# Kernel tuning notes

Hardware: AMD Instinct MI355X
Metric: run time of the kernel (lower is better)

## Reference

```python
import jax, jax.numpy as jnp
import numpy as np

HEADS = 20
HEAD_DIM = 64
NUM_IP = 20          # num_content_tokens (4) + num_style_tokens (16)
FU_SCALE = 0.5
STYLE_SCALE = 1.0
SCALE = 1.0 / np.sqrt(HEAD_DIM).astype(np.float32)


def setup_inputs() -> dict:
    key = jax.random.key(0)
    ks = jax.random.split(key, 9)
    B, S, H, C = 4, 4096, 1280, 2048
    T = 77 + NUM_IP  # text tokens + ip tokens
    w = 0.02
    return {
        "hidden_states": jax.random.normal(ks[0], (B, S, H), jnp.float32),
        "encoder_hidden_states": jax.random.normal(ks[1], (B, T, C), jnp.float32),
        "Wq": jax.random.normal(ks[2], (H, H), jnp.float32) * w,
        "Wk": jax.random.normal(ks[3], (H, C), jnp.float32) * w,
        "Wv": jax.random.normal(ks[4], (H, C), jnp.float32) * w,
        "Wk_ip": jax.random.normal(ks[5], (H, C), jnp.float32) * w,
        "Wv_ip": jax.random.normal(ks[6], (H, C), jnp.float32) * w,
        "Wo": jax.random.normal(ks[7], (H, H), jnp.float32) * w,
        "bo": jnp.zeros((H,), jnp.float32),
    }


def _to_heads(x):
    # [B, T, H] -> [B, heads, T, head_dim]
    B, T, _ = x.shape
    return x.reshape(B, T, HEADS, HEAD_DIM).transpose(0, 2, 1, 3)


def _blend(p):
    # cross-batch prob fusion: rows 1<-0, 3<-2 (CFG pairs)
    p = p.at[1].set(FU_SCALE * p[1] + (1.0 - FU_SCALE) * p[0])
    p = p.at[3].set(FU_SCALE * p[3] + (1.0 - FU_SCALE) * p[2])
    return p


def reference(hidden_states, encoder_hidden_states, Wq, Wk, Wv, Wk_ip, Wv_ip, Wo, bo):
    B, S, H = hidden_states.shape
    text = encoder_hidden_states[:, :-NUM_IP, :]   # [B, 77, C]
    ip = encoder_hidden_states[:, -NUM_IP:, :]     # [B, 20, C]

    q = _to_heads(hidden_states @ Wq.T)            # [B, h, S, d]
    k = _to_heads(text @ Wk.T)                     # [B, h, 77, d]
    v = _to_heads(text @ Wv.T)

    # fuAttn branch: explicit probs, blended across batch, then PV matmul
    probs = jax.nn.softmax(jnp.einsum('bhqd,bhkd->bhqk', q, k) * SCALE, axis=-1)
    probs = _blend(probs)
    raw = jnp.einsum('bhqk,bhkd->bhqd', probs, v)
    raw = raw.transpose(0, 2, 1, 3).reshape(B, S, H)

    # IP-adapter style cross-attention (fuIPAttn branch)
    ip_k = _to_heads(ip @ Wk_ip.T)                 # [B, h, 20, d]
    ip_v = _to_heads(ip @ Wv_ip.T)
    ip_probs = jax.nn.softmax(jnp.einsum('bhqd,bhkd->bhqk', q, ip_k) * SCALE, axis=-1)
    ip_probs = _blend(ip_probs)
    ip_hs = jnp.einsum('bhqk,bhkd->bhqd', ip_probs, ip_v)
    ip_hs = ip_hs.transpose(0, 2, 1, 3).reshape(B, S, H)

    hs = raw + STYLE_SCALE * ip_hs
    # batch rows 0 and 2 keep raw (text-only) attention output
    hs = hs.at[0].set(raw[0]).at[2].set(raw[2])

    # to_out[0] linear (bias) + to_out[1] dropout (identity at inference)
    return hs @ Wo.T + bo
```

## Files before the change

### kernel.cpp

```cpp
#include <hip/hip_runtime.h>
#include <cstdint>

typedef float floatx4 __attribute__((ext_vector_type(4)));
typedef __bf16 bf16x8 __attribute__((ext_vector_type(8)));

typedef const __attribute__((address_space(1))) void* gas_cvp;
typedef __attribute__((address_space(3))) void* las_vp;

__device__ __forceinline__ float bflo(unsigned int u) {
    return __builtin_bit_cast(float, u << 16);
}
__device__ __forceinline__ float bfhi(unsigned int u) {
    return __builtin_bit_cast(float, u & 0xffff0000u);
}
__device__ __forceinline__ unsigned short f2bf(float f) {
    unsigned int u = __builtin_bit_cast(unsigned int, f);
    u += 0x7fffu + ((u >> 16) & 1u);
    return (unsigned short)(u >> 16);
}
__device__ __forceinline__ bf16x8 ld8(const unsigned short* p) {
    return __builtin_bit_cast(bf16x8, *(const uint4*)p);
}
__device__ __forceinline__ floatx4 mfma32(bf16x8 a, bf16x8 b, floatx4 c) {
    return __builtin_amdgcn_mfma_f32_16x16x32_bf16(a, b, c, 0, 0, 0);
}
__device__ __forceinline__ void load_lds16(const void* g, void* l) {
    __builtin_amdgcn_global_load_lds(
        (gas_cvp)(unsigned long long)g,
        (las_vp)(unsigned int)(unsigned long long)l,
        16, 0, 0);
}

__global__ void cvt_f32_bf16(const float* __restrict__ in,
                             unsigned short* __restrict__ out, int n4) {
    int i = blockIdx.x * 256 + threadIdx.x;
    if (i < n4) {
        float4 v = ((const float4*)in)[i];
        ushort4 o;
        o.x = f2bf(v.x); o.y = f2bf(v.y); o.z = f2bf(v.z); o.w = f2bf(v.w);
        ((ushort4*)out)[i] = o;
    }
}

struct GemmJob {
    const unsigned short* A;
    const unsigned short* B;
    void* C;
    int M, N, K;
    int rpb, bstride, roff;
};
struct GemmArgs { GemmJob j[4]; };

template <bool F32OUT>
__global__ __launch_bounds__(256, 2) void gemm_bt(GemmArgs args,
                                                  const float* __restrict__ bias) {
    GemmJob jb = args.j[blockIdx.z];
    const int ntiles = jb.N >> 7;
    const int mtiles = (jb.M + 127) >> 7;

    int bx, by;
    {
        int idx = blockIdx.x;
        if ((mtiles & 7) == 0) {
            int gsz = ntiles * 8;
            int group = idx / gsz;
            int rem = idx - group * gsz;
            by = group * 8 + (rem & 7);
            bx = rem >> 3;
        } else {
            by = idx / ntiles;
            bx = idx - by * ntiles;
        }
    }
    if (by * 128 >= jb.M) return;

    const int tid  = threadIdx.x;
    const int lane = tid & 63;
    const int wid  = tid >> 6;
    const int K = jb.K, N = jb.N;

    __shared__ unsigned short ldsA[128 * 32];
    __shared__ unsigned short ldsB[128 * 32];

    const int colA = (tid & 3) * 8;
    auto maprow = [&](int r) -> size_t {
        r = (r < jb.M) ? r : (jb.M - 1);
        int b = r / jb.rpb;
        int t = r - b * jb.rpb;
        return (size_t)(b * jb.bstride + jb.roff + t);
    };
    const unsigned short* pa0 = jb.A + maprow(by * 128 + (tid >> 2)) * K + colA;
    const unsigned short* pa1 = jb.A + maprow(by * 128 + 64 + (tid >> 2)) * K + colA;
    const unsigned short* pb0 = jb.B + (size_t)(bx * 128 + (tid >> 2)) * K + colA;
    const unsigned short* pb1 = jb.B + (size_t)(bx * 128 + 64 + (tid >> 2)) * K + colA;

    unsigned short* la0 = &ldsA[tid * 8];
    unsigned short* la1 = &ldsA[2048 + tid * 8];
    unsigned short* lb0 = &ldsB[tid * 8];
    unsigned short* lb1 = &ldsB[2048 + tid * 8];

    floatx4 acc[4][4] = {};

    const int wm = (wid & 1) * 64;
    const int wn = (wid >> 1) * 64;
    const int fr = lane & 15;
    const int fc = (lane >> 4) * 8;

    for (int k0 = 0; k0 < K; k0 += 32) {
        __syncthreads();
        load_lds16(pa0 + k0, la0);
        load_lds16(pa1 + k0, la1);
        load_lds16(pb0 + k0, lb0);
        load_lds16(pb1 + k0, lb1);
        __syncthreads();

        bf16x8 af[4], bfv[4];
#pragma unroll
        for (int i = 0; i < 4; i++)
            af[i] = *(const bf16x8*)&ldsA[(wm + i * 16 + fr) * 32 + fc];
#pragma unroll
        for (int i = 0; i < 4; i++)
            bfv[i] = *(const bf16x8*)&ldsB[(wn + i * 16 + fr) * 32 + fc];
#pragma unroll
        for (int mi = 0; mi < 4; mi++)
#pragma unroll
            for (int ni = 0; ni < 4; ni++)
                acc[mi][ni] = __builtin_amdgcn_mfma_f32_16x16x32_bf16(
                    af[mi], bfv[ni], acc[mi][ni], 0, 0, 0);
    }

    const int colBase = bx * 128 + wn;
    const int rowBase = by * 128 + wm;
#pragma unroll
    for (int mi = 0; mi < 4; mi++) {
#pragma unroll
        for (int ni = 0; ni < 4; ni++) {
            int col  = colBase + ni * 16 + (lane & 15);
            int row0 = rowBase + mi * 16 + (lane >> 4) * 4;
#pragma unroll
            for (int r = 0; r < 4; r++) {
                int row = row0 + r;
                if (row < jb.M) {
                    float v = acc[mi][ni][r];
                    if (F32OUT)
                        ((float*)jb.C)[(size_t)row * N + col] = v + bias[col];
                    else
                        ((unsigned short*)jb.C)[(size_t)row * N + col] = f2bf(v);
                }
            }
        }
    }
}

#define NT 77
#define NI 20
#define VSTR 104
#define ISTR 40

__global__ __launch_bounds__(256, 2) void attn_mfma(
    const unsigned short* __restrict__ q,
    const unsigned short* __restrict__ kt,
    const unsigned short* __restrict__ vt,
    const unsigned short* __restrict__ kip,
    const unsigned short* __restrict__ vip,
    unsigned short* __restrict__ outp)
{
    const int tid = threadIdx.x;
    const int qt = blockIdx.x;
    const int h  = blockIdx.y;
    const int pz = blockIdx.z;
    const int b0 = 2 * pz;
    const int lane  = tid & 63;
    const int w     = tid >> 6;
    const int bi    = w >> 1;
    const int strip = (w & 1) * 16;
    const int fr = lane & 15;
    const int g  = lane >> 4;

    __shared__ unsigned short sVt[2][64][VSTR];
    __shared__ unsigned short sVipt[2][64][ISTR];
    __shared__ unsigned short sP[2][32][VSTR];

    for (int i = tid; i < 2 * 64 * (VSTR - NT); i += 256) {
        int b = i / (64 * (VSTR - NT)); int rem = i % (64 * (VSTR - NT));
        sVt[b][rem / (VSTR - NT)][NT + rem % (VSTR - NT)] = 0;
    }
    for (int i = tid; i < 2 * 64 * (ISTR - NI); i += 256) {
        int b = i / (64 * (ISTR - NI)); int rem = i % (64 * (ISTR - NI));
        sVipt[b][rem / (ISTR - NI)][NI + rem % (ISTR - NI)] = 0;
    }
    for (int i = tid; i < 2 * 32 * (VSTR - 80); i += 256) {
        int b = i / (32 * (VSTR - 80)); int rem = i % (32 * (VSTR - 80));
        sP[b][rem / (VSTR - 80)][80 + rem % (VSTR - 80)] = 0;
    }

    for (int c = tid; c < 2 * 8 * NT; c += 256) {
        int b = c / (8 * NT); int rem = c % (8 * NT);
        int dc = rem / NT; int key = rem % NT;
        uint4 v = *(const uint4*)&vt[((size_t)((b0 + b) * NT + key)) * 1280 + h * 64 + dc * 8];
        unsigned int uu[4] = {v.x, v.y, v.z, v.w};
#pragma unroll
        for (int j = 0; j < 4; j++) {
            sVt[b][dc * 8 + 2 * j][key]     = (unsigned short)(uu[j] & 0xffffu);
            sVt[b][dc * 8 + 2 * j + 1][key] = (unsigned short)(uu[j] >> 16);
        }
    }
    for (int c = tid; c < 2 * 8 * NI; c += 256) {
        int b = c / (8 * NI); int rem = c % (8 * NI);
        int dc = rem / NI; int key = rem % NI;
        uint4 v = *(const uint4*)&vip[((size_t)((b0 + b) * NI + key)) * 1280 + h * 64 + dc * 8];
        unsigned int uu[4] = {v.x, v.y, v.z, v.w};
#pragma unroll
        for (int j = 0; j < 4; j++) {
            sVipt[b][dc * 8 + 2 * j][key]     = (unsigned short)(uu[j] & 0xffffu);
            sVipt[b][dc * 8 + 2 * j + 1][key] = (unsigned short)(uu[j] >> 16);
        }
    }

    const size_t qbase = ((size_t)((b0 + bi) * 4096 + qt * 32 + strip + fr)) * 1280 + h * 64;
    bf16x8 aq0 = ld8(&q[qbase + g * 8]);
    bf16x8 aq1 = ld8(&q[qbase + 32 + g * 8]);

    floatx4 sc[5] = {};
#pragma unroll
    for (int t = 0; t < 5; t++) {
        int key = t * 16 + fr; key = (key < NT) ? key : (NT - 1);
        const size_t kb = ((size_t)((b0 + bi) * NT + key)) * 1280 + h * 64;
        sc[t] = mfma32(aq0, ld8(&kt[kb + g * 8]), sc[t]);
        sc[t] = mfma32(aq1, ld8(&kt[kb + 32 + g * 8]), sc[t]);
    }

#pragma unroll
    for (int r = 0; r < 4; r++) {
        float m = -1e30f;
#pragma unroll
        for (int t = 0; t < 5; t++) {
            float v = sc[t][r] * 0.125f;
            if (t == 4 && fr >= 13) v = -1e30f;
            sc[t][r] = v;
            m = fmaxf(m, v);
        }
        m = fmaxf(m, __shfl_xor(m, 1));
        m = fmaxf(m, __shfl_xor(m, 2));
        m = fmaxf(m, __shfl_xor(m, 4));
        m = fmaxf(m, __shfl_xor(m, 8));
        float sum = 0.f;
#pragma unroll
        for (int t = 0; t < 5; t++) {
            float e = __expf(sc[t][r] - m);
            sc[t][r] = e;
            sum += e;
        }
        sum += __shfl_xor(sum, 1);
        sum += __shfl_xor(sum, 2);
        sum += __shfl_xor(sum, 4);
        sum += __shfl_xor(sum, 8);
        float inv = 1.f / sum;
#pragma unroll
        for (int t = 0; t < 5; t++)
            sP[bi][strip + g * 4 + r][t * 16 + fr] = f2bf(sc[t][r] * inv);
    }
    __syncthreads();

    {
        unsigned int* p0 = (unsigned int*)&sP[0][0][0];
        unsigned int* p1 = (unsigned int*)&sP[1][0][0];
        for (int i = tid; i < 32 * VSTR / 2; i += 256) {
            unsigned int a = p0[i], b = p1[i];
            unsigned short r0 = f2bf(0.5f * (bflo(a) + bflo(b)));
            unsigned short r1 = f2bf(0.5f * (bfhi(a) + bfhi(b)));
            p1[i] = (unsigned int)r0 | ((unsigned int)r1 << 16);
        }
    }
    __syncthreads();

    floatx4 accO[4] = {};
    {
        const unsigned short* prow = &sP[bi][strip + fr][0];
        bf16x8 pa0 = ld8(prow + g * 8);
        bf16x8 pa1 = ld8(prow + 32 + g * 8);
        bf16x8 pa2 = ld8(prow + 64 + g * 8);
#pragma unroll
        for (int dt = 0; dt < 4; dt++) {
            const unsigned short* vrow = &sVt[bi][dt * 16 + fr][0];
            accO[dt] = mfma32(pa0, ld8(vrow + g * 8), accO[dt]);
            accO[dt] = mfma32(pa1, ld8(vrow + 32 + g * 8), accO[dt]);
            accO[dt] = mfma32(pa2, ld8(vrow + 64 + g * 8), accO[dt]);
        }
    }

    floatx4 si[2] = {};
#pragma unroll
    for (int t = 0; t < 2; t++) {
        int key = t * 16 + fr; key = (key < NI) ? key : (NI - 1);
        const size_t kb = ((size_t)((b0 + bi) * NI + key)) * 1280 + h * 64;
        si[t] = mfma32(aq0, ld8(&kip[kb + g * 8]), si[t]);
        si[t] = mfma32(aq1, ld8(&kip[kb + 32 + g * 8]), si[t]);
    }
#pragma unroll
    for (int r = 0; r < 4; r++) {
        float v0 = si[0][r] * 0.125f;
        float v1 = (fr >= 4) ? -1e30f : si[1][r] * 0.125f;
        float m = fmaxf(v0, v1);
        m = fmaxf(m, __shfl_xor(m, 1));
        m = fmaxf(m, __shfl_xor(m, 2));
        m = fmaxf(m, __shfl_xor(m, 4));
        m = fmaxf(m, __shfl_xor(m, 8));
        float e0 = __expf(v0 - m), e1 = __expf(v1 - m);
        float s = e0 + e1;
        s += __shfl_xor(s, 1);
        s += __shfl_xor(s, 2);
        s += __shfl_xor(s, 4);
        s += __shfl_xor(s, 8);
        float inv = 1.f / s;
        si[0][r] = e0 * inv;
        si[1][r] = e1 * inv;
    }
    __syncthreads();

#pragma unroll
    for (int r = 0; r < 4; r++) {
        sP[bi][strip + g * 4 + r][fr]      = f2bf(si[0][r]);
        sP[bi][strip + g * 4 + r][16 + fr] = f2bf(si[1][r]);
    }
    __syncthreads();

    for (int i = tid; i < 32 * 16; i += 256) {
        int r = i >> 4, kk = i & 15;
        unsigned int* p0 = (unsigned int*)&sP[0][r][0];
        unsigned int* p1 = (unsigned int*)&sP[1][r][0];
        unsigned int a = p0[kk], b = p1[kk];
        unsigned short r0 = f2bf(0.5f * (bflo(a) + bflo(b)));
        unsigned short r1 = f2bf(0.5f * (bfhi(a) + bfhi(b)));
        p1[kk] = (unsigned int)r0 | ((unsigned int)r1 << 16);
    }
    __syncthreads();

    if (bi == 1) {
        const unsigned short* prow = &sP[1][strip + fr][0];
        bf16x8 pip = ld8(prow + g * 8);
#pragma unroll
        for (int dt = 0; dt < 4; dt++)
            accO[dt] = mfma32(pip, ld8(&sVipt[1][dt * 16 + fr][g * 8]), accO[dt]);
    }

    const size_t orow0 = (size_t)((b0 + bi) * 4096 + qt * 32 + strip);
#pragma unroll
    for (int dt = 0; dt < 4; dt++) {
        int col = h * 64 + dt * 16 + fr;
#pragma unroll
        for (int r = 0; r < 4; r++)
            outp[(orow0 + g * 4 + r) * 1280 + col] = f2bf(accO[dt][r]);
    }
}

extern "C" void kernel_launch(void* const* d_in, const int* in_sizes, int n_in,
                              void* d_out, int out_size, void* d_ws, size_t ws_size,
                              hipStream_t stream) {
    const float* hs   = (const float*)d_in[0];
    const float* ehs  = (const float*)d_in[1];
    const float* Wq   = (const float*)d_in[2];
    const float* Wk   = (const float*)d_in[3];
    const float* Wv   = (const float*)d_in[4];
    const float* Wkip = (const float*)d_in[5];
    const float* Wvip = (const float*)d_in[6];
    const float* Wo   = (const float*)d_in[7];
    const float* bo   = (const float*)d_in[8];

    char* w = (char*)d_ws;
    size_t off = 0;
    auto alloc = [&](size_t bytes) {
        char* pp = w + off;
        off += (bytes + 255) & ~(size_t)255;
        return pp;
    };
    unsigned short* hs_bf   = (unsigned short*)alloc(16384ull * 1280 * 2);
    unsigned short* q_bf    = (unsigned short*)alloc(16384ull * 1280 * 2);
    unsigned short* at_bf   = (unsigned short*)alloc(16384ull * 1280 * 2);
    unsigned short* ehs_bf  = (unsigned short*)alloc(4ull * 97 * 2048 * 2);
    unsigned short* Wq_bf   = (unsigned short*)alloc(1280ull * 1280 * 2);
    unsigned short* Wk_bf   = (unsigned short*)alloc(1280ull * 2048 * 2);
    unsigned short* Wv_bf   = (unsigned short*)alloc(1280ull * 2048 * 2);
    unsigned short* Wkip_bf = (unsigned short*)alloc(1280ull * 2048 * 2);
    unsigned short* Wvip_bf = (unsigned short*)alloc(1280ull * 2048 * 2);
    unsigned short* Wo_bf   = (unsigned short*)alloc(1280ull * 1280 * 2);
    unsigned short* kt  = (unsigned short*)alloc(308ull * 1280 * 2);
    unsigned short* vt  = (unsigned short*)alloc(308ull * 1280 * 2);
    unsigned short* kip = (unsigned short*)alloc(80ull * 1280 * 2);
    unsigned short* vip = (unsigned short*)alloc(80ull * 1280 * 2);

    auto cvt = [&](const float* src, unsigned short* dst, size_t n) {
        int n4 = (int)(n / 4);
        cvt_f32_bf16<<<dim3((n4 + 255) / 256), dim3(256), 0, stream>>>(src, dst, n4);
    };
    cvt(hs,   hs_bf,   16384ull * 1280);
    cvt(ehs,  ehs_bf,  4ull * 97 * 2048);
    cvt(Wq,   Wq_bf,   1280ull * 1280);
    cvt(Wk,   Wk_bf,   1280ull * 2048);
    cvt(Wv,   Wv_bf,   1280ull * 2048);
    cvt(Wkip, Wkip_bf, 1280ull * 2048);
    cvt(Wvip, Wvip_bf, 1280ull * 2048);
    cvt(Wo,   Wo_bf,   1280ull * 1280);

    GemmArgs gq{};
    gq.j[0] = GemmJob{hs_bf, Wq_bf, (void*)q_bf, 16384, 1280, 1280, 16384, 0, 0};
    gemm_bt<false><<<dim3(1280, 1, 1), 256, 0, stream>>>(gq, nullptr);

    GemmArgs gkv{};
    gkv.j[0] = GemmJob{ehs_bf, Wk_bf,   (void*)kt,  308, 1280, 2048, 77, 97, 0};
    gkv.j[1] = GemmJob{ehs_bf, Wv_bf,   (void*)vt,  308, 1280, 2048, 77, 97, 0};
    gkv.j[2] = GemmJob{ehs_bf, Wkip_bf, (void*)kip,  80, 1280, 2048, 20, 97, 77};
    gkv.j[3] = GemmJob{ehs_bf, Wvip_bf, (void*)vip,  80, 1280, 2048, 20, 97, 77};
    gemm_bt<false><<<dim3(30, 1, 4), 256, 0, stream>>>(gkv, nullptr);

    attn_mfma<<<dim3(128, 20, 2), 256, 0, stream>>>(q_bf, kt, vt, kip, vip, at_bf);

    GemmArgs go{};
    go.j[0] = GemmJob{at_bf, Wo_bf, d_out, 16384, 1280, 1280, 16384, 0, 0};
    gemm_bt<true><<<dim3(1280, 1, 1), 256, 0, stream>>>(go, bo);
}
```

Before: 488.6 us.

## Swizzle GEMM LDS layout and batch conversion and projection launches

Applies an XOR swizzle to the LDS column layout in the bf16 GEMM so fragment reads avoid bank conflicts. Merges the seven small fp32-to-bf16 conversions into one multi-job launch. Folds the K/V/IP projection GEMMs into the Q projection launch via a fifth grid z-slice, which cuts launch count. The cost is many early-exiting blocks in the small-job z slices (1280 blocks each) and a wider kernel argument struct.

```diff
diff --git a/kernel.cpp b/kernel.cpp
--- a/kernel.cpp
+++ b/kernel.cpp
@@ -42,6 +42,20 @@
     }
 }
 
+struct CvtJob { const float* src; unsigned short* dst; int n4; };
+struct CvtJobs { CvtJob j[7]; };
+
+__global__ void cvt_multi(CvtJobs jobs) {
+    CvtJob jb = jobs.j[blockIdx.y];
+    int i = blockIdx.x * 256 + threadIdx.x;
+    if (i < jb.n4) {
+        float4 v = ((const float4*)jb.src)[i];
+        ushort4 o;
+        o.x = f2bf(v.x); o.y = f2bf(v.y); o.z = f2bf(v.z); o.w = f2bf(v.w);
+        ((ushort4*)jb.dst)[i] = o;
+    }
+}
+
 struct GemmJob {
     const unsigned short* A;
     const unsigned short* B;
@@ -49,7 +63,7 @@
     int M, N, K;
     int rpb, bstride, roff;
 };
-struct GemmArgs { GemmJob j[4]; };
+struct GemmArgs { GemmJob j[5]; };
 
 template <bool F32OUT>
 __global__ __launch_bounds__(256, 2) void gemm_bt(GemmArgs args,
@@ -82,7 +96,7 @@
     __shared__ unsigned short ldsA[128 * 32];
     __shared__ unsigned short ldsB[128 * 32];
 
-    const int colA = (tid & 3) * 8;
+    const int colA = (((tid & 3) ^ ((tid >> 3) & 3)) * 8);
     auto maprow = [&](int r) -> size_t {
         r = (r < jb.M) ? r : (jb.M - 1);
         int b = r / jb.rpb;
@@ -104,7 +118,8 @@
     const int wm = (wid & 1) * 64;
     const int wn = (wid >> 1) * 64;
     const int fr = lane & 15;
-    const int fc = (lane >> 4) * 8;
+    const int g  = lane >> 4;
+    const int fcs = (g ^ ((fr >> 1) & 3)) * 8;
 
     for (int k0 = 0; k0 < K; k0 += 32) {
         __syncthreads();
@@ -117,10 +132,10 @@
         bf16x8 af[4], bfv[4];
 #pragma unroll
         for (int i = 0; i < 4; i++)
-            af[i] = *(const bf16x8*)&ldsA[(wm + i * 16 + fr) * 32 + fc];
+            af[i] = *(const bf16x8*)&ldsA[(wm + i * 16 + fr) * 32 + fcs];
 #pragma unroll
         for (int i = 0; i < 4; i++)
-            bfv[i] = *(const bf16x8*)&ldsB[(wn + i * 16 + fr) * 32 + fc];
+            bfv[i] = *(const bf16x8*)&ldsB[(wn + i * 16 + fr) * 32 + fcs];
 #pragma unroll
         for (int mi = 0; mi < 4; mi++)
 #pragma unroll
@@ -135,8 +150,8 @@
     for (int mi = 0; mi < 4; mi++) {
 #pragma unroll
         for (int ni = 0; ni < 4; ni++) {
-            int col  = colBase + ni * 16 + (lane & 15);
-            int row0 = rowBase + mi * 16 + (lane >> 4) * 4;
+            int col  = colBase + ni * 16 + fr;
+            int row0 = rowBase + mi * 16 + g * 4;
 #pragma unroll
             for (int r = 0; r < 4; r++) {
                 int row = row0 + r;
@@ -389,29 +404,25 @@
     unsigned short* kip = (unsigned short*)alloc(80ull * 1280 * 2);
     unsigned short* vip = (unsigned short*)alloc(80ull * 1280 * 2);
 
-    auto cvt = [&](const float* src, unsigned short* dst, size_t n) {
-        int n4 = (int)(n / 4);
-        cvt_f32_bf16<<<dim3((n4 + 255) / 256), dim3(256), 0, stream>>>(src, dst, n4);
-    };
-    cvt(hs,   hs_bf,   16384ull * 1280);
-    cvt(ehs,  ehs_bf,  4ull * 97 * 2048);
-    cvt(Wq,   Wq_bf,   1280ull * 1280);
-    cvt(Wk,   Wk_bf,   1280ull * 2048);
-    cvt(Wv,   Wv_bf,   1280ull * 2048);
-    cvt(Wkip, Wkip_bf, 1280ull * 2048);
-    cvt(Wvip, Wvip_bf, 1280ull * 2048);
-    cvt(Wo,   Wo_bf,   1280ull * 1280);
+    cvt_f32_bf16<<<dim3(20480, 1, 1), 256, 0, stream>>>(hs, hs_bf, 16384 * 1280 / 4);
+
+    CvtJobs cj{};
+    cj.j[0] = CvtJob{ehs,  ehs_bf,  (int)(4ull * 97 * 2048 / 4)};
+    cj.j[1] = CvtJob{Wq,   Wq_bf,   1280 * 1280 / 4};
+    cj.j[2] = CvtJob{Wk,   Wk_bf,   1280 * 2048 / 4};
+    cj.j[3] = CvtJob{Wv,   Wv_bf,   1280 * 2048 / 4};
+    cj.j[4] = CvtJob{Wkip, Wkip_bf, 1280 * 2048 / 4};
+    cj.j[5] = CvtJob{Wvip, Wvip_bf, 1280 * 2048 / 4};
+    cj.j[6] = CvtJob{Wo,   Wo_bf,   1280 * 1280 / 4};
+    cvt_multi<<<dim3(2560, 7, 1), 256, 0, stream>>>(cj);
 
     GemmArgs gq{};
-    gq.j[0] = GemmJob{hs_bf, Wq_bf, (void*)q_bf, 16384, 1280, 1280, 16384, 0, 0};
-    gemm_bt<false><<<dim3(1280, 1, 1), 256, 0, stream>>>(gq, nullptr);
-
-    GemmArgs gkv{};
-    gkv.j[0] = GemmJob{ehs_bf, Wk_bf,   (void*)kt,  308, 1280, 2048, 77, 97, 0};
-    gkv.j[1] = GemmJob{ehs_bf, Wv_bf,   (void*)vt,  308, 1280, 2048, 77, 97, 0};
-    gkv.j[2] = GemmJob{ehs_bf, Wkip_bf, (void*)kip,  80, 1280, 2048, 20, 97, 77};
-    gkv.j[3] = GemmJob{ehs_bf, Wvip_bf, (void*)vip,  80, 1280, 2048, 20, 97, 77};
-    gemm_bt<false><<<dim3(30, 1, 4), 256, 0, stream>>>(gkv, nullptr);
+    gq.j[0] = GemmJob{hs_bf,  Wq_bf,   (void*)q_bf, 16384, 1280, 1280, 16384, 0, 0};
+    gq.j[1] = GemmJob{ehs_bf, Wk_bf,   (void*)kt,     308, 1280, 2048, 77, 97, 0};
+    gq.j[2] = GemmJob{ehs_bf, Wv_bf,   (void*)vt,     308, 1280, 2048, 77, 97, 0};
+    gq.j[3] = GemmJob{ehs_bf, Wkip_bf, (void*)kip,     80, 1280, 2048, 20, 97, 77};
+    gq.j[4] = GemmJob{ehs_bf, Wvip_bf, (void*)vip,     80, 1280, 2048, 20, 97, 77};
+    gemm_bt<false><<<dim3(1280, 1, 5), 256, 0, stream>>>(gq, nullptr);
 
     attn_mfma<<<dim3(128, 20, 2), 256, 0, stream>>>(q_bf, kt, vt, kip, vip, at_bf);
 
```

Measured after the change: 453.0 us. 1.08x faster.
